# Kernel optimization log

Hardware: AMD Instinct MI355X
Metric: run time of the kernel (lower is better)

Reference implementation:

```python
import jax, jax.numpy as jnp
import numpy as np

FEATURES = 32
RES = 512
TIME_DIM = 16
N_PTS = 1048576


def _sample_plane(plane, gx, gy):
    """Bilinear grid_sample, align_corners=True.
    plane: (C, H, W); gx in [-1,1] indexes W, gy in [-1,1] indexes H.
    Returns (N, C).
    """
    C, H, W = plane.shape
    ix = (gx + 1.0) * 0.5 * (W - 1)
    iy = (gy + 1.0) * 0.5 * (H - 1)
    ix0f = jnp.clip(jnp.floor(ix), 0, W - 1)
    iy0f = jnp.clip(jnp.floor(iy), 0, H - 1)
    ix0 = ix0f.astype(jnp.int32)
    iy0 = iy0f.astype(jnp.int32)
    ix1 = jnp.minimum(ix0 + 1, W - 1)
    iy1 = jnp.minimum(iy0 + 1, H - 1)
    wx = ix - ix0f  # (N,)
    wy = iy - iy0f
    v00 = plane[:, iy0, ix0]  # (C, N)
    v01 = plane[:, iy0, ix1]
    v10 = plane[:, iy1, ix0]
    v11 = plane[:, iy1, ix1]
    out = (v00 * ((1 - wx) * (1 - wy)) + v01 * (wx * (1 - wy))
           + v10 * ((1 - wx) * wy) + v11 * (wx * wy))
    return out.T  # (N, C)


def setup_inputs() -> dict:
    key = jax.random.key(0)
    ks = jax.random.split(key, 7)
    x = jax.random.uniform(ks[0], (N_PTS, 4), dtype=jnp.float32, minval=-1.0, maxval=1.0)
    plane_xy = jax.random.normal(ks[1], (FEATURES, RES, RES), dtype=jnp.float32)
    plane_xz = jax.random.normal(ks[2], (FEATURES, RES, RES), dtype=jnp.float32)
    plane_yz = jax.random.normal(ks[3], (FEATURES, RES, RES), dtype=jnp.float32)
    plane_xt = jax.random.normal(ks[4], (FEATURES, RES, TIME_DIM), dtype=jnp.float32)
    plane_yt = jax.random.normal(ks[5], (FEATURES, RES, TIME_DIM), dtype=jnp.float32)
    plane_zt = jax.random.normal(ks[6], (FEATURES, RES, TIME_DIM), dtype=jnp.float32)
    return {"x": x, "plane_xy": plane_xy, "plane_xz": plane_xz, "plane_yz": plane_yz,
            "plane_xt": plane_xt, "plane_yt": plane_yt, "plane_zt": plane_zt}


def reference(x, plane_xy, plane_xz, plane_yz, plane_xt, plane_yt, plane_zt):
    center, scale = 0.0, 2.0
    u = (x - center) / scale + 0.5   # map to [0,1]
    g = u * 2.0 - 1.0                # back to [-1,1] grid coords
    gx, gy, gz, gt = g[:, 0], g[:, 1], g[:, 2], g[:, 3]
    feat_xy = _sample_plane(plane_xy, gx, gy)
    feat_xz = _sample_plane(plane_xz, gx, gz)
    feat_yz = _sample_plane(plane_yz, gy, gz)
    feat_xt = _sample_plane(plane_xt, gx, gt)
    feat_yt = _sample_plane(plane_yt, gy, gt)
    feat_zt = _sample_plane(plane_zt, gz, gt)
    return jnp.concatenate([feat_xy, feat_xz, feat_yz, feat_xt, feat_yt, feat_zt], axis=1)
```

## Files before the change

### kernel.cpp

```cpp
#include <hip/hip_runtime.h>
#include <stdint.h>

#define NPTS 1048576
#define NBINS 32768

using u16x8 = __attribute__((ext_vector_type(8))) unsigned short;
using f32x4 = __attribute__((ext_vector_type(4))) float;

#define OFF_HIST     51904512ul
#define OFF_CURSOR   52035584ul
#define OFF_KEYS     52166656ul
#define OFF_XS       54263808ul
#define OFF_PID      71041024ul
#define WS_NEED_FULL 75235328ul
#define WS_NEED_MID  51904512ul

__device__ __forceinline__ float bf2f(unsigned short u) {
    union { unsigned int i; float f; } c; c.i = ((unsigned int)u) << 16; return c.f;
}
__device__ __forceinline__ unsigned int f2bf_bits(float f) {
    union { float f; unsigned int i; } c; c.f = f;
    unsigned int i = c.i;
    i += 0x7fffu + ((i >> 16) & 1u);
    return i >> 16;
}
__device__ __forceinline__ unsigned int spread3(unsigned int v) {
    v &= 31u;
    v = (v | (v << 8)) & 0x100Fu;
    v = (v | (v << 4)) & 0x10C3u;
    v = (v | (v << 2)) & 0x1249u;
    return v;
}

template<int WC, int H, int W>
__global__ __launch_bounds__(256) void transpose3(const float* __restrict__ s0,
                                                  const float* __restrict__ s1,
                                                  const float* __restrict__ s2,
                                                  unsigned short* __restrict__ dst) {
    __shared__ float tile[32][WC + 1];
    const float* src = (blockIdx.y == 0) ? s0 : (blockIdx.y == 1) ? s1 : s2;
    constexpr int CH = W / WC;
    const int h  = blockIdx.x / CH;
    const int w0 = (blockIdx.x % CH) * WC;
    const int HW = H * W;
    const float* s = src + h * W + w0;
    for (int i = threadIdx.x; i < 32 * WC; i += 256) {
        int c = i / WC, w = i - c * WC;
        tile[c][w] = s[c * HW + w];
    }
    __syncthreads();
    unsigned int* d = (unsigned int*)(dst + (size_t)blockIdx.y * HW * 32
                                          + (size_t)(h * W + w0) * 32);
    for (int i = threadIdx.x; i < 16 * WC; i += 256) {
        int w = i >> 4, cp = i & 15;
        unsigned int lo = f2bf_bits(tile[cp * 2][w]);
        unsigned int hi = f2bf_bits(tile[cp * 2 + 1][w]);
        d[i] = lo | (hi << 16);
    }
}

__global__ __launch_bounds__(256) void hist_kernel(const float* __restrict__ x,
                                                   unsigned int* __restrict__ hist,
                                                   unsigned short* __restrict__ keys) {
    int p = blockIdx.x * 256 + threadIdx.x;
    f32x4 xv = *(const f32x4*)(x + (size_t)p * 4);
    int bx = min(31, max(0, (int)((xv[0] + 1.0f) * 16.0f)));
    int by = min(31, max(0, (int)((xv[1] + 1.0f) * 16.0f)));
    int bz = min(31, max(0, (int)((xv[2] + 1.0f) * 16.0f)));
    unsigned int key = (spread3(bx) << 2) | (spread3(by) << 1) | spread3(bz);
    keys[p] = (unsigned short)key;
    atomicAdd(&hist[key], 1u);
}

__global__ __launch_bounds__(1024) void scan_kernel(const unsigned int* __restrict__ hist,
                                                    unsigned int* __restrict__ cursor) {
    __shared__ unsigned int part[1024];
    int t = threadIdx.x;
    unsigned int local[32];
    unsigned int s = 0;
    int base = t * 32;
#pragma unroll
    for (int j = 0; j < 32; ++j) { local[j] = s; s += hist[base + j]; }
    part[t] = s;
    __syncthreads();
    for (int off = 1; off < 1024; off <<= 1) {
        unsigned int v = 0;
        if (t >= off) v = part[t - off];
        __syncthreads();
        if (t >= off) part[t] += v;
        __syncthreads();
    }
    unsigned int chunkbase = part[t] - s;
#pragma unroll
    for (int j = 0; j < 32; ++j) cursor[base + j] = chunkbase + local[j];
}

__global__ __launch_bounds__(256) void scatter_kernel(const float* __restrict__ x,
                                                      const unsigned short* __restrict__ keys,
                                                      unsigned int* __restrict__ cursor,
                                                      f32x4* __restrict__ xs,
                                                      unsigned int* __restrict__ pid) {
    int p = blockIdx.x * 256 + threadIdx.x;
    f32x4 xv = *(const f32x4*)(x + (size_t)p * 4);
    unsigned int k = keys[p];
    unsigned int pos = atomicAdd(&cursor[k], 1u);
    xs[pos] = xv;
    pid[pos] = (unsigned int)p;
}

template<int W, int H, bool NT>
__device__ __forceinline__ void sample_one(const unsigned short* __restrict__ pl,
                                           float gw, float gh, int sub,
                                           float* __restrict__ o) {
    float ix = (gw + 1.0f) * 0.5f * (float)(W - 1);
    float iy = (gh + 1.0f) * 0.5f * (float)(H - 1);
    float fx0 = fminf(fmaxf(floorf(ix), 0.0f), (float)(W - 1));
    float fy0 = fminf(fmaxf(floorf(iy), 0.0f), (float)(H - 1));
    int ix0 = (int)fx0, iy0 = (int)fy0;
    int ix1 = min(ix0 + 1, W - 1), iy1 = min(iy0 + 1, H - 1);
    float wx = ix - fx0, wy = iy - fy0;
    float wx0 = 1.0f - wx, wy0 = 1.0f - wy;
    float w00 = wx0 * wy0, w01 = wx * wy0, w10 = wx0 * wy, w11 = wx * wy;
    const int base = sub * 8;
    u16x8 v00 = *(const u16x8*)(pl + ((iy0 * W + ix0) * 32 + base));
    u16x8 v01 = *(const u16x8*)(pl + ((iy0 * W + ix1) * 32 + base));
    u16x8 v10 = *(const u16x8*)(pl + ((iy1 * W + ix0) * 32 + base));
    u16x8 v11 = *(const u16x8*)(pl + ((iy1 * W + ix1) * 32 + base));
    f32x4 r0, r1;
#pragma unroll
    for (int j = 0; j < 4; ++j)
        r0[j] = bf2f(v00[j]) * w00 + bf2f(v01[j]) * w01
              + bf2f(v10[j]) * w10 + bf2f(v11[j]) * w11;
#pragma unroll
    for (int j = 0; j < 4; ++j)
        r1[j] = bf2f(v00[4 + j]) * w00 + bf2f(v01[4 + j]) * w01
              + bf2f(v10[4 + j]) * w10 + bf2f(v11[4 + j]) * w11;
    if (NT) {
        __builtin_nontemporal_store(r0, (f32x4*)(o));
        __builtin_nontemporal_store(r1, (f32x4*)(o + 4));
    } else {
        *(f32x4*)(o)     = r0;
        *(f32x4*)(o + 4) = r1;
    }
}

__device__ __forceinline__ void sample_all(f32x4 xv, int sub,
                                           const unsigned short* __restrict__ ws,
                                           float* __restrict__ o) {
    float gx = (xv[0] * 0.5f + 0.5f) * 2.0f - 1.0f;
    float gy = (xv[1] * 0.5f + 0.5f) * 2.0f - 1.0f;
    float gz = (xv[2] * 0.5f + 0.5f) * 2.0f - 1.0f;
    float gt = (xv[3] * 0.5f + 0.5f) * 2.0f - 1.0f;
    sample_one<512, 512, true>(ws + 0ul,        gx, gy, sub, o + 0);
    sample_one<512, 512, true>(ws + 8388608ul,  gx, gz, sub, o + 32);
    sample_one<512, 512, true>(ws + 16777216ul, gy, gz, sub, o + 64);
    sample_one<16,  512, true>(ws + 25165824ul, gx, gt, sub, o + 96);
    sample_one<16,  512, true>(ws + 25427968ul, gy, gt, sub, o + 128);
    sample_one<16,  512, true>(ws + 25690112ul, gz, gt, sub, o + 160);
}

__global__ __launch_bounds__(256) void sample_sorted(const f32x4* __restrict__ xs,
                                                     const unsigned int* __restrict__ pid,
                                                     const unsigned short* __restrict__ ws,
                                                     float* __restrict__ out) {
    int nwg = gridDim.x;
    int cpx = nwg >> 3;
    int bid = blockIdx.x;
    int swz = (bid & 7) * cpx + (bid >> 3);
    int tid = swz * 256 + threadIdx.x;
    int s   = tid >> 2;
    int sub = tid & 3;
    f32x4 xv = xs[s];
    int p = pid[s];
    sample_all(xv, sub, ws, out + (size_t)p * 192 + sub * 8);
}

__global__ __launch_bounds__(256) void sample_kernel(const float* __restrict__ x,
                                                     const unsigned short* __restrict__ ws,
                                                     float* __restrict__ out) {
    int tid = blockIdx.x * 256 + threadIdx.x;
    int p   = tid >> 2;
    int sub = tid & 3;
    f32x4 xv = *(const f32x4*)(x + (size_t)p * 4);
    sample_all(xv, sub, ws, out + (size_t)p * 192 + sub * 8);
}

template<int W, int H>
__device__ __forceinline__ void sample_direct_one(const float* __restrict__ pl,
                                                  float gw, float gh, int sub,
                                                  float* __restrict__ o) {
    float ix = (gw + 1.0f) * 0.5f * (float)(W - 1);
    float iy = (gh + 1.0f) * 0.5f * (float)(H - 1);
    float fx0 = fminf(fmaxf(floorf(ix), 0.0f), (float)(W - 1));
    float fy0 = fminf(fmaxf(floorf(iy), 0.0f), (float)(H - 1));
    int ix0 = (int)fx0, iy0 = (int)fy0;
    int ix1 = min(ix0 + 1, W - 1), iy1 = min(iy0 + 1, H - 1);
    float wx = ix - fx0, wy = iy - fy0;
    float wx0 = 1.0f - wx, wy0 = 1.0f - wy;
    float w00 = wx0 * wy0, w01 = wx * wy0, w10 = wx0 * wy, w11 = wx * wy;
    const int HW = W * H;
    int a00 = iy0 * W + ix0, a01 = iy0 * W + ix1;
    int a10 = iy1 * W + ix0, a11 = iy1 * W + ix1;
    const float* b = pl + (size_t)sub * 8 * HW;
#pragma unroll
    for (int j = 0; j < 8; ++j) {
        o[j] = b[a00] * w00 + b[a01] * w01 + b[a10] * w10 + b[a11] * w11;
        b += HW;
    }
}

__global__ __launch_bounds__(256) void sample_fallback(const float* __restrict__ x,
    const float* __restrict__ pxy, const float* __restrict__ pxz,
    const float* __restrict__ pyz, const float* __restrict__ pxt,
    const float* __restrict__ pyt, const float* __restrict__ pzt,
    float* __restrict__ out) {
    int tid = blockIdx.x * 256 + threadIdx.x;
    int p   = tid >> 2;
    int sub = tid & 3;
    f32x4 xv = *(const f32x4*)(x + (size_t)p * 4);
    float gx = (xv[0] * 0.5f + 0.5f) * 2.0f - 1.0f;
    float gy = (xv[1] * 0.5f + 0.5f) * 2.0f - 1.0f;
    float gz = (xv[2] * 0.5f + 0.5f) * 2.0f - 1.0f;
    float gt = (xv[3] * 0.5f + 0.5f) * 2.0f - 1.0f;
    float* o = out + (size_t)p * 192 + sub * 8;
    sample_direct_one<512, 512>(pxy, gx, gy, sub, o + 0);
    sample_direct_one<512, 512>(pxz, gx, gz, sub, o + 32);
    sample_direct_one<512, 512>(pyz, gy, gz, sub, o + 64);
    sample_direct_one<16,  512>(pxt, gx, gt, sub, o + 96);
    sample_direct_one<16,  512>(pyt, gy, gt, sub, o + 128);
    sample_direct_one<16,  512>(pzt, gz, gt, sub, o + 160);
}

extern "C" void kernel_launch(void* const* d_in, const int* in_sizes, int n_in,
                              void* d_out, int out_size, void* d_ws, size_t ws_size,
                              hipStream_t stream) {
    const float* x   = (const float*)d_in[0];
    const float* pxy = (const float*)d_in[1];
    const float* pxz = (const float*)d_in[2];
    const float* pyz = (const float*)d_in[3];
    const float* pxt = (const float*)d_in[4];
    const float* pyt = (const float*)d_in[5];
    const float* pzt = (const float*)d_in[6];
    float* out = (float*)d_out;

    if (ws_size >= WS_NEED_FULL) {
        char* wsb = (char*)d_ws;
        unsigned short* planes = (unsigned short*)wsb;
        unsigned int*   hist   = (unsigned int*)(wsb + OFF_HIST);
        unsigned int*   cursor = (unsigned int*)(wsb + OFF_CURSOR);
        unsigned short* keys   = (unsigned short*)(wsb + OFF_KEYS);
        f32x4*          xs     = (f32x4*)(wsb + OFF_XS);
        unsigned int*   pid    = (unsigned int*)(wsb + OFF_PID);

        hipMemsetAsync(hist, 0, NBINS * sizeof(unsigned int), stream);
        transpose3<64, 512, 512><<<dim3(512 * 8, 3), 256, 0, stream>>>(pxy, pxz, pyz, planes);
        transpose3<16, 512, 16><<<dim3(512, 3), 256, 0, stream>>>(pxt, pyt, pzt, planes + 25165824ul);
        hist_kernel<<<NPTS / 256, 256, 0, stream>>>(x, hist, keys);
        scan_kernel<<<1, 1024, 0, stream>>>(hist, cursor);
        scatter_kernel<<<NPTS / 256, 256, 0, stream>>>(x, keys, cursor, xs, pid);
        sample_sorted<<<(NPTS * 4) / 256, 256, 0, stream>>>(xs, pid, planes, out);
    } else if (ws_size >= WS_NEED_MID) {
        unsigned short* planes = (unsigned short*)d_ws;
        transpose3<64, 512, 512><<<dim3(512 * 8, 3), 256, 0, stream>>>(pxy, pxz, pyz, planes);
        transpose3<16, 512, 16><<<dim3(512, 3), 256, 0, stream>>>(pxt, pyt, pzt, planes + 25165824ul);
        sample_kernel<<<(NPTS * 4) / 256, 256, 0, stream>>>(x, planes, out);
    } else {
        sample_fallback<<<(NPTS * 4) / 256, 256, 0, stream>>>(x, pxy, pxz, pyz, pxt, pyt, pzt, out);
    }
}
```

Before: 372.6 us.

## Split sorted sampling into three passes, one big plane each

Replaces the single sorted sampling kernel, which gathered from all six planes, with three kernel passes. Each pass samples one 512x512 plane plus one time plane, so the working set per pass is one 16 MB bf16 plane and has a better chance of staying in L2/MALL cache. The cost is reading the sorted points and ids three times, three launches instead of one, and output rows being written in three scattered partial pieces.

```diff
diff --git a/kernel.cpp b/kernel.cpp
--- a/kernel.cpp
+++ b/kernel.cpp
@@ -14,6 +14,13 @@
 #define OFF_PID      71041024ul
 #define WS_NEED_FULL 75235328ul
 #define WS_NEED_MID  51904512ul
+
+#define PL_XY 0ul
+#define PL_XZ 8388608ul
+#define PL_YZ 16777216ul
+#define PL_XT 25165824ul
+#define PL_YT 25427968ul
+#define PL_ZT 25690112ul
 
 __device__ __forceinline__ float bf2f(unsigned short u) {
     union { unsigned int i; float f; } c; c.i = ((unsigned int)u) << 16; return c.f;
@@ -144,6 +151,29 @@
     }
 }
 
+template<size_t BIGOFF, size_t TOFF, int L0, int L1, int LT, int OUT1, int OUT2>
+__global__ __launch_bounds__(256) void sample_pass(const f32x4* __restrict__ xs,
+                                                   const unsigned int* __restrict__ pid,
+                                                   const unsigned short* __restrict__ planes,
+                                                   float* __restrict__ out) {
+    int cpx = gridDim.x >> 3;
+    int bid = blockIdx.x;
+    int swz = (bid & 7) * cpx + (bid >> 3);
+    int tid = swz * 256 + threadIdx.x;
+    int s   = tid >> 2;
+    int sub = tid & 3;
+    f32x4 v = xs[s];
+    unsigned int p = pid[s];
+    p = min(p, (unsigned int)(NPTS - 1));
+    float g0 = (v[L0] * 0.5f + 0.5f) * 2.0f - 1.0f;
+    float g1 = (v[L1] * 0.5f + 0.5f) * 2.0f - 1.0f;
+    float gw = (v[LT] * 0.5f + 0.5f) * 2.0f - 1.0f;
+    float gt = (v[3]  * 0.5f + 0.5f) * 2.0f - 1.0f;
+    float* o = out + (size_t)p * 192 + sub * 8;
+    sample_one<512, 512, true>(planes + BIGOFF, g0, g1, sub, o + OUT1);
+    sample_one<16,  512, true>(planes + TOFF,   gw, gt, sub, o + OUT2);
+}
+
 __device__ __forceinline__ void sample_all(f32x4 xv, int sub,
                                            const unsigned short* __restrict__ ws,
                                            float* __restrict__ o) {
@@ -151,28 +181,12 @@
     float gy = (xv[1] * 0.5f + 0.5f) * 2.0f - 1.0f;
     float gz = (xv[2] * 0.5f + 0.5f) * 2.0f - 1.0f;
     float gt = (xv[3] * 0.5f + 0.5f) * 2.0f - 1.0f;
-    sample_one<512, 512, true>(ws + 0ul,        gx, gy, sub, o + 0);
-    sample_one<512, 512, true>(ws + 8388608ul,  gx, gz, sub, o + 32);
-    sample_one<512, 512, true>(ws + 16777216ul, gy, gz, sub, o + 64);
-    sample_one<16,  512, true>(ws + 25165824ul, gx, gt, sub, o + 96);
-    sample_one<16,  512, true>(ws + 25427968ul, gy, gt, sub, o + 128);
-    sample_one<16,  512, true>(ws + 25690112ul, gz, gt, sub, o + 160);
-}
-
-__global__ __launch_bounds__(256) void sample_sorted(const f32x4* __restrict__ xs,
-                                                     const unsigned int* __restrict__ pid,
-                                                     const unsigned short* __restrict__ ws,
-                                                     float* __restrict__ out) {
-    int nwg = gridDim.x;
-    int cpx = nwg >> 3;
-    int bid = blockIdx.x;
-    int swz = (bid & 7) * cpx + (bid >> 3);
-    int tid = swz * 256 + threadIdx.x;
-    int s   = tid >> 2;
-    int sub = tid & 3;
-    f32x4 xv = xs[s];
-    int p = pid[s];
-    sample_all(xv, sub, ws, out + (size_t)p * 192 + sub * 8);
+    sample_one<512, 512, true>(ws + PL_XY, gx, gy, sub, o + 0);
+    sample_one<512, 512, true>(ws + PL_XZ, gx, gz, sub, o + 32);
+    sample_one<512, 512, true>(ws + PL_YZ, gy, gz, sub, o + 64);
+    sample_one<16,  512, true>(ws + PL_XT, gx, gt, sub, o + 96);
+    sample_one<16,  512, true>(ws + PL_YT, gy, gt, sub, o + 128);
+    sample_one<16,  512, true>(ws + PL_ZT, gz, gt, sub, o + 160);
 }
 
 __global__ __launch_bounds__(256) void sample_kernel(const float* __restrict__ x,
@@ -254,15 +268,17 @@
 
         hipMemsetAsync(hist, 0, NBINS * sizeof(unsigned int), stream);
         transpose3<64, 512, 512><<<dim3(512 * 8, 3), 256, 0, stream>>>(pxy, pxz, pyz, planes);
-        transpose3<16, 512, 16><<<dim3(512, 3), 256, 0, stream>>>(pxt, pyt, pzt, planes + 25165824ul);
+        transpose3<16, 512, 16><<<dim3(512, 3), 256, 0, stream>>>(pxt, pyt, pzt, planes + PL_XT);
         hist_kernel<<<NPTS / 256, 256, 0, stream>>>(x, hist, keys);
         scan_kernel<<<1, 1024, 0, stream>>>(hist, cursor);
         scatter_kernel<<<NPTS / 256, 256, 0, stream>>>(x, keys, cursor, xs, pid);
-        sample_sorted<<<(NPTS * 4) / 256, 256, 0, stream>>>(xs, pid, planes, out);
+        sample_pass<PL_XY, PL_XT, 0, 1, 0, 0,  96><<<(NPTS * 4) / 256, 256, 0, stream>>>(xs, pid, planes, out);
+        sample_pass<PL_XZ, PL_ZT, 0, 2, 2, 32, 160><<<(NPTS * 4) / 256, 256, 0, stream>>>(xs, pid, planes, out);
+        sample_pass<PL_YZ, PL_YT, 1, 2, 1, 64, 128><<<(NPTS * 4) / 256, 256, 0, stream>>>(xs, pid, planes, out);
     } else if (ws_size >= WS_NEED_MID) {
         unsigned short* planes = (unsigned short*)d_ws;
         transpose3<64, 512, 512><<<dim3(512 * 8, 3), 256, 0, stream>>>(pxy, pxz, pyz, planes);
-        transpose3<16, 512, 16><<<dim3(512, 3), 256, 0, stream>>>(pxt, pyt, pzt, planes + 25165824ul);
+        transpose3<16, 512, 16><<<dim3(512, 3), 256, 0, stream>>>(pxt, pyt, pzt, planes + PL_XT);
         sample_kernel<<<(NPTS * 4) / 256, 256, 0, stream>>>(x, planes, out);
     } else {
         sample_fallback<<<(NPTS * 4) / 256, 256, 0, stream>>>(x, pxy, pxz, pyz, pxt, pyt, pzt, out);
```

Result: faster. 359.5 us (-3.5%).
